# Performance work log

Measured on AMD Instinct MI355X. Metric: run time of the kernel, lower is better.

Reference implementation:

```python
import jax, jax.numpy as jnp
import numpy as np

B, K, N, M = 4, 512, 4096, 4
CHI2_95 = 7.815   # chi-square df=3, q=0.95
JITTER = 1e-6
ALPHA = 1.5       # sigma_cover_alpha
SIG_FLOOR = 1e-3
SIG_CEIL = 100.0
BETA = 0.85       # beta_parent_sigma
SHRINK = 1.0      # parent_sigma_shrink
KNN = 8           # fps_knn


def _sym(A):
    return 0.5 * (A + jnp.swapaxes(A, -1, -2))


def _chol3(S, eps=1e-6):
    # manual 3x3 Cholesky (vectorized, never fails), mirrors _safe_cholesky_3x3_manual
    s00, s11, s22 = S[..., 0, 0], S[..., 1, 1], S[..., 2, 2]
    s01, s02, s12 = S[..., 0, 1], S[..., 0, 2], S[..., 1, 2]
    l00 = jnp.sqrt(jnp.clip(s00, eps))
    l10 = s01 / jnp.clip(l00, eps)
    l20 = s02 / jnp.clip(l00, eps)
    l11 = jnp.sqrt(jnp.clip(s11 - l10 ** 2, eps))
    l21 = (s12 - l20 * l10) / jnp.clip(l11, eps)
    l22 = jnp.sqrt(jnp.clip(s22 - l20 ** 2 - l21 ** 2, eps))
    zz = jnp.zeros_like(l00)
    return jnp.stack([jnp.stack([l00, zz, zz], -1),
                      jnp.stack([l10, l11, zz], -1),
                      jnp.stack([l20, l21, l22], -1)], -2)


def _allocate_quota(pi, n_total, mask):
    # vectorized version of _allocate_quota: floor + largest-remainder
    valid = mask > 0.5
    pi = jnp.where(valid, pi, 0.0)
    pi = pi / jnp.clip(jnp.sum(pi, -1, keepdims=True), 1e-9)
    raw = pi * float(n_total)
    base = jnp.floor(raw)
    rem = (float(n_total) - jnp.sum(base, -1)).astype(jnp.int32)          # [B]
    frac = jnp.where(valid, raw - base, -1e9)
    order = jnp.argsort(-frac, axis=-1)
    rank = jnp.argsort(order, axis=-1)
    n_k = base.astype(jnp.int32) + (rank < rem[:, None]).astype(jnp.int32)
    return jnp.where(valid, n_k, 0)


def setup_inputs() -> dict:
    key = jax.random.key(0)
    k1, k2, k3, k4 = jax.random.split(key, 4)
    mu_p = jax.random.normal(k1, (B, K, 3), jnp.float32) * 5.0
    A = jax.random.normal(k2, (B, K, 3, 3), jnp.float32)
    Sig_p = 0.1 * jnp.einsum('bkij,bklj->bkil', A, A) + 0.5 * jnp.eye(3, dtype=jnp.float32)
    occ = jax.random.uniform(k3, (B, K), jnp.float32) + 0.1
    mask_parent = jnp.ones((B, K), jnp.float32)
    node_mask = jnp.ones((B, N), jnp.float32)
    z = jax.random.normal(k4, (B, N, M, 3), jnp.float32)
    return {"mu_p": mu_p, "Sig_p": Sig_p, "occ": occ,
            "mask_parent": mask_parent, "node_mask": node_mask, "z": z}


def reference(mu_p, Sig_p, occ, mask_parent, node_mask, z):
    b, k, _ = mu_p.shape
    n = node_mask.shape[1]
    m = z.shape[2]
    I3 = jnp.eye(3, dtype=mu_p.dtype)

    # --- quota allocation ---
    pi = occ * (mask_parent > 0.5).astype(occ.dtype)
    n_k = _allocate_quota(pi, n, mask_parent)                              # [B,K]

    # --- child -> parent assignment (packed layout, replaces Python loops) ---
    csum = jnp.cumsum(n_k, -1)                                             # [B,K]
    ar = jnp.arange(n)
    parent_idx = jax.vmap(lambda c: jnp.searchsorted(c, ar, side='right'))(csum)
    parent_idx = jnp.clip(parent_idx, 0, k - 1)                            # [B,N]

    # --- sample inside parent ellipsoid (rejection-lite) ---
    Sig_s = _sym(Sig_p * SHRINK) + JITTER * I3
    mu_c = jax.vmap(lambda a, i: a[i])(mu_p, parent_idx)                   # [B,N,3]
    Sig_c = jax.vmap(lambda a, i: a[i])(Sig_s, parent_idx)                 # [B,N,3,3]
    L = _chol3(Sig_c)                                                      # [B,N,3,3]
    cand = mu_c[:, :, None, :] + jnp.einsum('bnij,bnmj->bnmi', L, z)       # [B,N,M,3]
    # delta = cand - mu = L z, so maha2 = z^T z exactly (as in the torch code)
    maha2 = jnp.sum(z * z, -1)                                             # [B,N,M]
    inside = maha2 <= CHI2_95
    # keep first inside candidate; else smallest maha2
    score = jnp.where(inside, jnp.arange(m, dtype=maha2.dtype), 1e6 + maha2)
    pick = jnp.argmin(score, axis=-1)                                      # [B,N]
    mu0 = jnp.take_along_axis(cand, pick[..., None, None], axis=2)[:, :, 0, :]
    mu0 = mu0 * node_mask[..., None]                                       # [B,N,3]

    # --- spacing-based Sigma (kNN mean distance, isotropic) ---
    sq = jnp.sum(mu0 * mu0, -1)
    d2 = sq[:, :, None] + sq[:, None, :] - 2.0 * jnp.einsum('bnd,bmd->bnm', mu0, mu0)
    pair_ok = (node_mask[:, :, None] > 0.5) & (node_mask[:, None, :] > 0.5)
    eye = jnp.eye(n, dtype=bool)
    d2 = jnp.where(pair_ok & ~eye, d2, 1e9)
    neg_top, _ = jax.lax.top_k(-d2, KNN)                                   # [B,N,KNN]
    d_mean = jnp.mean(jnp.sqrt(jnp.clip(-neg_top, 0.0)), -1)               # [B,N]
    sigma = jnp.clip(ALPHA * d_mean, SIG_FLOOR, SIG_CEIL)
    Sig_spacing = (sigma ** 2)[..., None, None] * I3 + JITTER * I3         # [B,N,3,3]

    # --- parent/spacing Sigma blend ---
    Sig_pc = jax.vmap(lambda a, i: a[i])(_sym(Sig_p), parent_idx)
    Sig_pc = _sym(Sig_pc) + JITTER * I3
    Sig0 = BETA * Sig_pc + (1.0 - BETA) * Sig_spacing
    Sig0 = _sym(Sig0) + JITTER * I3
    Sig0 = Sig0 * node_mask[:, :, None, None]
    return mu0, Sig0, parent_idx
```

## Files before the change

### kernel.cpp

```cpp
#include <hip/hip_runtime.h>
#include <math.h>

#define B_ 4
#define K_ 512
#define N_ 4096
#define M_ 4

#define KTHREADS 512
#define SLOTS 8
#define SEGS 64
#define ROWS 16
#define CHUNK 1024
#define NCHUNK (N_ / CHUNK)
#define BIGF 3.0e38f

#define CSW(x,y) { float _lo = fminf(x,y); y = fmaxf(x,y); x = _lo; }

#define SORT8S(s0,s1,s2,s3,s4,s5,s6,s7) \
    CSW(s0,s1) CSW(s2,s3) CSW(s4,s5) CSW(s6,s7) \
    CSW(s0,s2) CSW(s1,s3) CSW(s4,s6) CSW(s5,s7) \
    CSW(s1,s2) CSW(s5,s6) \
    CSW(s0,s4) CSW(s1,s5) CSW(s2,s6) CSW(s3,s7) \
    CSW(s2,s4) CSW(s3,s5) \
    CSW(s1,s2) CSW(s3,s4) CSW(s5,s6)

#define BMERGE8S(K0,K1,K2,K3,K4,K5,K6,K7, S0,S1,S2,S3,S4,S5,S6,S7) \
    K0 = fminf(K0,S7); K1 = fminf(K1,S6); K2 = fminf(K2,S5); K3 = fminf(K3,S4); \
    K4 = fminf(K4,S3); K5 = fminf(K5,S2); K6 = fminf(K6,S1); K7 = fminf(K7,S0); \
    CSW(K0,K4) CSW(K1,K5) CSW(K2,K6) CSW(K3,K7) \
    CSW(K0,K2) CSW(K1,K3) CSW(K4,K6) CSW(K5,K7) \
    CSW(K0,K1) CSW(K2,K3) CSW(K4,K5) CSW(K6,K7)

#define WMERGE(K0,K1,K2,K3,K4,K5,K6,K7, off) { \
    float _b0 = __shfl_xor(K0, off, 64); float _b1 = __shfl_xor(K1, off, 64); \
    float _b2 = __shfl_xor(K2, off, 64); float _b3 = __shfl_xor(K3, off, 64); \
    float _b4 = __shfl_xor(K4, off, 64); float _b5 = __shfl_xor(K5, off, 64); \
    float _b6 = __shfl_xor(K6, off, 64); float _b7 = __shfl_xor(K7, off, 64); \
    BMERGE8S(K0,K1,K2,K3,K4,K5,K6,K7, _b0,_b1,_b2,_b3,_b4,_b5,_b6,_b7) }

__global__ __launch_bounds__(512) void fused_kernel(const float* __restrict__ mu_p,
                                                    const float* __restrict__ Sig_p,
                                                    const float* __restrict__ occ,
                                                    const float* __restrict__ mask_parent,
                                                    const float* __restrict__ node_mask,
                                                    const float* __restrict__ z,
                                                    float* __restrict__ out,
                                                    float4* __restrict__ mu4,
                                                    int useF4)
{
    __shared__ double sh_a[K_];
    __shared__ double sh_part[32];
    __shared__ alignas(16) double sh_frac[K_];
    __shared__ alignas(16) float  sh_ffr[K_];
    __shared__ float  csf[K_];
    __shared__ double Lsh[K_][6];
    __shared__ int    sh_wsum[8];
    __shared__ double s_S;
    __shared__ int    s_rem;

    int b  = blockIdx.x >> 3;
    int rb = blockIdx.x & 7;
    int k  = threadIdx.x;

    float mk = mask_parent[b * K_ + k];
    bool valid = mk > 0.5f;
    double pi = valid ? (double)occ[b * K_ + k] : 0.0;
    sh_a[k] = pi;
    __syncthreads();

    if (k < 32) {
        const double* a = sh_a + (k >> 3) * 128;
        int j = k & 7;
        double r = a[j];
        for (int i = 8; i < 128; i += 8) r += a[j + i];
        sh_part[k] = r;
    }
    __syncthreads();
    if (k == 0) {
        double pw[4];
        #pragma unroll
        for (int blk = 0; blk < 4; ++blk) {
            const double* p = sh_part + blk * 8;
            pw[blk] = ((p[0]+p[1])+(p[2]+p[3]))+((p[4]+p[5])+(p[6]+p[7]));
        }
        s_S = fmax((pw[0]+pw[1])+(pw[2]+pw[3]), 1e-9);
    }
    __syncthreads();

    double raw  = (pi / s_S) * 4096.0;
    double base = floor(raw);
    double frac = valid ? (raw - base) : -1e9;
    sh_frac[k] = frac;
    sh_ffr[k]  = (float)frac;
    __syncthreads();
    sh_a[k] = base;
    __syncthreads();
    if (k < 32) {
        const double* a = sh_a + (k >> 3) * 128;
        int j = k & 7;
        double r = a[j];
        for (int i = 8; i < 128; i += 8) r += a[j + i];
        sh_part[k] = r;
    }
    __syncthreads();
    if (k == 0) {
        double pw[4];
        #pragma unroll
        for (int blk = 0; blk < 4; ++blk) {
            const double* p = sh_part + blk * 8;
            pw[blk] = ((p[0]+p[1])+(p[2]+p[3]))+((p[4]+p[5])+(p[6]+p[7]));
        }
        s_rem = (int)(4096.0 - ((pw[0]+pw[1])+(pw[2]+pw[3])));
    }
    __syncthreads();

    int nkv = 0;
    if (valid) {
        float fl = (float)frac;
        int rank = 0, eq = 0;
        const float4* f4 = reinterpret_cast<const float4*>(sh_ffr);
        #pragma unroll 4
        for (int j4 = 0; j4 < K_ / 4; ++j4) {
            float4 q = f4[j4];
            rank += (q.x > fl) ? 1 : 0;  eq += (q.x == fl) ? 1 : 0;
            rank += (q.y > fl) ? 1 : 0;  eq += (q.y == fl) ? 1 : 0;
            rank += (q.z > fl) ? 1 : 0;  eq += (q.z == fl) ? 1 : 0;
            rank += (q.w > fl) ? 1 : 0;  eq += (q.w == fl) ? 1 : 0;
        }
        if (__builtin_expect(eq != 1, 0)) {
            double f = frac;
            rank = 0;
            for (int j = 0; j < K_; ++j) {
                double fj = sh_frac[j];
                rank += ((fj > f) || (fj == f && j < k)) ? 1 : 0;
            }
        }
        nkv = (int)base + (rank < s_rem ? 1 : 0);
    }

    {
        int lane = k & 63;
        int w    = k >> 6;
        int v = nkv;
        #pragma unroll
        for (int off = 1; off < 64; off <<= 1) {
            int t = __shfl_up(v, off, 64);
            v += (lane >= off) ? t : 0;
        }
        if (lane == 63) sh_wsum[w] = v;
        __syncthreads();
        int woff = 0;
        #pragma unroll
        for (int i = 0; i < 7; ++i) woff += (i < w) ? sh_wsum[i] : 0;
        csf[k] = (float)(v + woff);
    }

    {
        const float* S = Sig_p + (size_t)(b * K_ + k) * 9;
        double s00 = (double)S[0] + 1e-6;
        double s01 = 0.5 * ((double)S[1] + (double)S[3]);
        double s02 = 0.5 * ((double)S[2] + (double)S[6]);
        double s11 = (double)S[4] + 1e-6;
        double s12 = 0.5 * ((double)S[5] + (double)S[7]);
        double s22 = (double)S[8] + 1e-6;

        const double eps = 1e-6;
        double l00 = sqrt(fmax(s00, eps));
        double l10 = s01 / fmax(l00, eps);
        double l20 = s02 / fmax(l00, eps);
        double l11 = sqrt(fmax(s11 - l10 * l10, eps));
        double l21 = (s12 - l20 * l10) / fmax(l11, eps);
        double l22 = sqrt(fmax(s22 - l20 * l20 - l21 * l21, eps));

        Lsh[k][0] = l00; Lsh[k][1] = l10; Lsh[k][2] = l20;
        Lsh[k][3] = l11; Lsh[k][4] = l21; Lsh[k][5] = l22;
    }
    __syncthreads();

    int n = rb * 512 + k;
    float nf = (float)n;
    int lo = 0, hi = K_;
    while (lo < hi) {
        int mid = (lo + hi) >> 1;
        if (csf[mid] <= nf) lo = mid + 1; else hi = mid;
    }
    int p = lo < (K_ - 1) ? lo : (K_ - 1);

    double l00 = Lsh[p][0], l10 = Lsh[p][1], l20 = Lsh[p][2];
    double l11 = Lsh[p][3], l21 = Lsh[p][4], l22 = Lsh[p][5];

    const float* zp = z + (size_t)(b * N_ + n) * (M_ * 3);
    double bestScore = 1e30;
    int pick = 0;
    #pragma unroll
    for (int m = 0; m < M_; ++m) {
        double z0 = (double)zp[m*3+0], z1 = (double)zp[m*3+1], z2 = (double)zp[m*3+2];
        double maha2 = (z0 * z0 + z1 * z1) + z2 * z2;
        double score = (maha2 <= 7.815) ? (double)m : (1e6 + maha2);
        if (score < bestScore) { bestScore = score; pick = m; }
    }

    double z0 = (double)zp[pick*3+0], z1 = (double)zp[pick*3+1], z2 = (double)zp[pick*3+2];
    const float* mu = mu_p + (size_t)(b * K_ + p) * 3;
    double nm = (double)node_mask[b * N_ + n];
    double c0 = ((double)mu[0] + ((l00 * z0)))                       * nm;
    double c1 = ((double)mu[1] + ((l10 * z0 + l11 * z1)))            * nm;
    double c2 = ((double)mu[2] + ((l20 * z0 + l21 * z1) + l22 * z2)) * nm;

    size_t o = (size_t)(b * N_ + n) * 3;
    float f0 = (float)c0, f1 = (float)c1, f2 = (float)c2;
    out[o + 0] = f0;
    out[o + 1] = f1;
    out[o + 2] = f2;
    if (useF4) {
        float sq = (f0 * f0 + f1 * f1) + f2 * f2;
        mu4[b * N_ + n] = make_float4(f0, f1, f2, sq);
    }
    out[(size_t)B_ * N_ * 12 + (size_t)(b * N_ + n)] = (float)p;
}

#define LOADU_G(u, SQ) { \
    int col_ = colbase + u * SEGS + seg; \
    float4 q_ = cp[col_]; \
    s##u = fmaf(a00, q_.x, fmaf(a01, q_.y, fmaf(a02, q_.z, q_.w))); \
    r##u = fmaf(a10, q_.x, fmaf(a11, q_.y, fmaf(a12, q_.z, q_.w))); \
    if (SQ) { \
        s##u = (col_ == n0) ? BIGF : s##u; \
        r##u = (col_ == n1) ? BIGF : r##u; } }

#define LOADU_S(u, SQ) { \
    int col_ = colbase + u * SEGS + seg; \
    size_t o_ = (size_t)(bN + col_) * 3; \
    float qx_ = mu0[o_], qy_ = mu0[o_+1], qz_ = mu0[o_+2]; \
    float qw_ = (qx_*qx_ + qy_*qy_) + qz_*qz_; \
    s##u = fmaf(a00, qx_, fmaf(a01, qy_, fmaf(a02, qz_, qw_))); \
    r##u = fmaf(a10, qx_, fmaf(a11, qy_, fmaf(a12, qz_, qw_))); \
    if (SQ) { \
        s##u = (col_ == n0) ? BIGF : s##u; \
        r##u = (col_ == n1) ? BIGF : r##u; } }

#define GROUP8(LD, SQ) { \
    float s0,s1,s2,s3,s4,s5,s6,s7, r0,r1,r2,r3,r4,r5,r6,r7; \
    LD(0,SQ) LD(1,SQ) LD(2,SQ) LD(3,SQ) \
    LD(4,SQ) LD(5,SQ) LD(6,SQ) LD(7,SQ) \
    SORT8S(s0,s1,s2,s3,s4,s5,s6,s7) \
    BMERGE8S(ka0,ka1,ka2,ka3,ka4,ka5,ka6,ka7, s0,s1,s2,s3,s4,s5,s6,s7) \
    SORT8S(r0,r1,r2,r3,r4,r5,r6,r7) \
    BMERGE8S(kb0,kb1,kb2,kb3,kb4,kb5,kb6,kb7, r0,r1,r2,r3,r4,r5,r6,r7) }

__global__ __launch_bounds__(KTHREADS, 4) void knn_kernel(const float* __restrict__ Sig_p,
                                                          const float* __restrict__ node_mask,
                                                          const float4* __restrict__ mu4,
                                                          int useF4,
                                                          float* __restrict__ out)
{
    __shared__ float  shk[ROWS][8 * 8 + 1];

    int b   = blockIdx.x / (N_ / ROWS);
    int rb  = blockIdx.x % (N_ / ROWS);
    int tid = threadIdx.x;
    int slot = tid & (SLOTS - 1);
    int seg  = tid >> 3;

    const float* mu0 = out;
    const float4* cp = mu4 + (size_t)b * N_;
    int bN = b * N_;
    int n0 = rb * ROWS + slot;
    int n1 = n0 + SLOTS;

    float x0, y0, z0v, x1, y1, z1v;
    if (useF4) {
        float4 p0 = cp[n0]; x0 = p0.x; y0 = p0.y; z0v = p0.z;
        float4 p1 = cp[n1]; x1 = p1.x; y1 = p1.y; z1v = p1.z;
    } else {
        size_t so0 = (size_t)(bN + n0) * 3;
        size_t so1 = (size_t)(bN + n1) * 3;
        x0 = mu0[so0]; y0 = mu0[so0+1]; z0v = mu0[so0+2];
        x1 = mu0[so1]; y1 = mu0[so1+1]; z1v = mu0[so1+2];
    }
    float a00 = -2.0f*x0, a01 = -2.0f*y0, a02 = -2.0f*z0v;
    float a10 = -2.0f*x1, a11 = -2.0f*y1, a12 = -2.0f*z1v;

    float ka0=BIGF,ka1=BIGF,ka2=BIGF,ka3=BIGF,ka4=BIGF,ka5=BIGF,ka6=BIGF,ka7=BIGF;
    float kb0=BIGF,kb1=BIGF,kb2=BIGF,kb3=BIGF,kb4=BIGF,kb5=BIGF,kb6=BIGF,kb7=BIGF;

    int selfc = (rb * ROWS) >> 10;

    if (useF4) {
        #pragma unroll
        for (int c = 0; c < NCHUNK; ++c) {
            if (c == selfc) {
                { int colbase = c * CHUNK;       GROUP8(LOADU_G, 1) }
                { int colbase = c * CHUNK + 512; GROUP8(LOADU_G, 1) }
            } else {
                { int colbase = c * CHUNK;       GROUP8(LOADU_G, 0) }
                { int colbase = c * CHUNK + 512; GROUP8(LOADU_G, 0) }
            }
        }
    } else {
        #pragma unroll
        for (int c = 0; c < NCHUNK; ++c) {
            if (c == selfc) {
                { int colbase = c * CHUNK;       GROUP8(LOADU_S, 1) }
                { int colbase = c * CHUNK + 512; GROUP8(LOADU_S, 1) }
            } else {
                { int colbase = c * CHUNK;       GROUP8(LOADU_S, 0) }
                { int colbase = c * CHUNK + 512; GROUP8(LOADU_S, 0) }
            }
        }
    }

    WMERGE(ka0,ka1,ka2,ka3,ka4,ka5,ka6,ka7, 8)
    WMERGE(ka0,ka1,ka2,ka3,ka4,ka5,ka6,ka7, 16)
    WMERGE(ka0,ka1,ka2,ka3,ka4,ka5,ka6,ka7, 32)
    WMERGE(kb0,kb1,kb2,kb3,kb4,kb5,kb6,kb7, 8)
    WMERGE(kb0,kb1,kb2,kb3,kb4,kb5,kb6,kb7, 16)
    WMERGE(kb0,kb1,kb2,kb3,kb4,kb5,kb6,kb7, 32)

    int lane = tid & 63;
    int w    = tid >> 6;
    if (lane < SLOTS) {
        shk[lane][w*8+0] = ka0; shk[lane][w*8+1] = ka1;
        shk[lane][w*8+2] = ka2; shk[lane][w*8+3] = ka3;
        shk[lane][w*8+4] = ka4; shk[lane][w*8+5] = ka5;
        shk[lane][w*8+6] = ka6; shk[lane][w*8+7] = ka7;
        shk[lane+SLOTS][w*8+0] = kb0; shk[lane+SLOTS][w*8+1] = kb1;
        shk[lane+SLOTS][w*8+2] = kb2; shk[lane+SLOTS][w*8+3] = kb3;
        shk[lane+SLOTS][w*8+4] = kb4; shk[lane+SLOTS][w*8+5] = kb5;
        shk[lane+SLOTS][w*8+6] = kb6; shk[lane+SLOTS][w*8+7] = kb7;
    }
    __syncthreads();

    if (tid < ROWS) {
        int r = tid;
        int nn = rb * ROWS + r;
        float e0=BIGF,e1=BIGF,e2=BIGF,e3=BIGF,e4=BIGF,e5=BIGF,e6=BIGF,e7=BIGF;
        #pragma unroll
        for (int w2 = 0; w2 < 8; ++w2) {
            float b0 = shk[r][w2*8+0], b1 = shk[r][w2*8+1];
            float b2 = shk[r][w2*8+2], b3 = shk[r][w2*8+3];
            float b4 = shk[r][w2*8+4], b5 = shk[r][w2*8+5];
            float b6 = shk[r][w2*8+6], b7 = shk[r][w2*8+7];
            BMERGE8S(e0,e1,e2,e3,e4,e5,e6,e7, b0,b1,b2,b3,b4,b5,b6,b7)
        }

        float cn;
        if (useF4) {
            cn = cp[nn].w;
        } else {
            size_t so = (size_t)(bN + nn) * 3;
            float xx = mu0[so], yy = mu0[so+1], zz = mu0[so+2];
            cn = (xx*xx + yy*yy) + zz*zz;
        }

        double s0 = sqrt(fmax((double)(cn + e0), 0.0)), s1 = sqrt(fmax((double)(cn + e1), 0.0));
        double s2 = sqrt(fmax((double)(cn + e2), 0.0)), s3 = sqrt(fmax((double)(cn + e3), 0.0));
        double s4 = sqrt(fmax((double)(cn + e4), 0.0)), s5 = sqrt(fmax((double)(cn + e5), 0.0));
        double s6 = sqrt(fmax((double)(cn + e6), 0.0)), s7 = sqrt(fmax((double)(cn + e7), 0.0));
        double d_mean = (((s0 + s1) + (s2 + s3)) + ((s4 + s5) + (s6 + s7))) / 8.0;

        double sigma = fmin(fmax(1.5 * d_mean, 1e-3), 100.0);
        double spacing = sigma * sigma + 1e-6;

        int p = (int)out[(size_t)B_ * N_ * 12 + (size_t)(bN + nn)];
        const float* S = Sig_p + (size_t)(b * K_ + p) * 9;
        double s00 = (double)S[0];
        double s01 = 0.5 * ((double)S[1] + (double)S[3]);
        double s02 = 0.5 * ((double)S[2] + (double)S[6]);
        double s11 = (double)S[4];
        double s12 = 0.5 * ((double)S[5] + (double)S[7]);
        double s22 = (double)S[8];

        const double BETA = 0.85;
        const double OMB  = 1.0 - 0.85;
        double nm = (double)node_mask[bN + nn];

        double d00 = (BETA * (s00 + 1e-6) + OMB * spacing) + 1e-6;
        double d11 = (BETA * (s11 + 1e-6) + OMB * spacing) + 1e-6;
        double d22 = (BETA * (s22 + 1e-6) + OMB * spacing) + 1e-6;
        double o01 = BETA * s01;
        double o02 = BETA * s02;
        double o12 = BETA * s12;

        float* Sg = out + (size_t)B_ * N_ * 3 + (size_t)(bN + nn) * 9;
        Sg[0] = (float)(d00 * nm); Sg[1] = (float)(o01 * nm); Sg[2] = (float)(o02 * nm);
        Sg[3] = (float)(o01 * nm); Sg[4] = (float)(d11 * nm); Sg[5] = (float)(o12 * nm);
        Sg[6] = (float)(o02 * nm); Sg[7] = (float)(o12 * nm); Sg[8] = (float)(d22 * nm);
    }
}

extern "C" void kernel_launch(void* const* d_in, const int* in_sizes, int n_in,
                              void* d_out, int out_size, void* d_ws, size_t ws_size,
                              hipStream_t stream)
{
    const float* mu_p        = (const float*)d_in[0];
    const float* Sig_p       = (const float*)d_in[1];
    const float* occ         = (const float*)d_in[2];
    const float* mask_parent = (const float*)d_in[3];
    const float* node_mask   = (const float*)d_in[4];
    const float* z           = (const float*)d_in[5];
    float* out = (float*)d_out;

    int useF4 = (ws_size >= (size_t)B_ * N_ * sizeof(float4)) ? 1 : 0;
    float4* mu4 = (float4*)d_ws;

    fused_kernel<<<B_ * 8, 512, 0, stream>>>(mu_p, Sig_p, occ, mask_parent,
                                             node_mask, z, out, mu4, useF4);
    knn_kernel<<<B_ * (N_ / ROWS), KTHREADS, 0, stream>>>(Sig_p, node_mask,
                                                          mu4, useF4, out);
}
```

Before: 47.15 us.

## Process four query rows per thread in kNN kernel to reuse candidate loads

Each thread now keeps top-8 lists for four query points instead of two, so every float4 candidate load feeds four distance computations. This doubles rows per block and halves the block count. The chunk loop is no longer unrolled, probably to limit code size and register growth. The cost is higher register pressure from 32 running top-k registers plus temporaries, which may cut occupancy under launch_bounds(512,4) or cause spills, and fewer blocks reduce parallelism.

New measurement: 56.90 us. +20.7%, slower.

```diff
diff --git a/kernel.cpp b/kernel.cpp
--- a/kernel.cpp
+++ b/kernel.cpp
@@ -9,7 +9,7 @@
 #define KTHREADS 512
 #define SLOTS 8
 #define SEGS 64
-#define ROWS 16
+#define ROWSB 32
 #define CHUNK 1024
 #define NCHUNK (N_ / CHUNK)
 #define BIGF 3.0e38f
@@ -219,34 +219,49 @@
     out[(size_t)B_ * N_ * 12 + (size_t)(b * N_ + n)] = (float)p;
 }
 
-#define LOADU_G(u, SQ) { \
+#define LOADU4_G(u, SQ) { \
     int col_ = colbase + u * SEGS + seg; \
     float4 q_ = cp[col_]; \
-    s##u = fmaf(a00, q_.x, fmaf(a01, q_.y, fmaf(a02, q_.z, q_.w))); \
-    r##u = fmaf(a10, q_.x, fmaf(a11, q_.y, fmaf(a12, q_.z, q_.w))); \
+    qa##u = fmaf(a00, q_.x, fmaf(a01, q_.y, fmaf(a02, q_.z, q_.w))); \
+    qb##u = fmaf(a10, q_.x, fmaf(a11, q_.y, fmaf(a12, q_.z, q_.w))); \
+    qc##u = fmaf(a20, q_.x, fmaf(a21, q_.y, fmaf(a22, q_.z, q_.w))); \
+    qd##u = fmaf(a30, q_.x, fmaf(a31, q_.y, fmaf(a32, q_.z, q_.w))); \
     if (SQ) { \
-        s##u = (col_ == n0) ? BIGF : s##u; \
-        r##u = (col_ == n1) ? BIGF : r##u; } }
-
-#define LOADU_S(u, SQ) { \
+        qa##u = (col_ == n0) ? BIGF : qa##u; \
+        qb##u = (col_ == n1) ? BIGF : qb##u; \
+        qc##u = (col_ == n2) ? BIGF : qc##u; \
+        qd##u = (col_ == n3) ? BIGF : qd##u; } }
+
+#define LOADU4_S(u, SQ) { \
     int col_ = colbase + u * SEGS + seg; \
     size_t o_ = (size_t)(bN + col_) * 3; \
     float qx_ = mu0[o_], qy_ = mu0[o_+1], qz_ = mu0[o_+2]; \
     float qw_ = (qx_*qx_ + qy_*qy_) + qz_*qz_; \
-    s##u = fmaf(a00, qx_, fmaf(a01, qy_, fmaf(a02, qz_, qw_))); \
-    r##u = fmaf(a10, qx_, fmaf(a11, qy_, fmaf(a12, qz_, qw_))); \
+    qa##u = fmaf(a00, qx_, fmaf(a01, qy_, fmaf(a02, qz_, qw_))); \
+    qb##u = fmaf(a10, qx_, fmaf(a11, qy_, fmaf(a12, qz_, qw_))); \
+    qc##u = fmaf(a20, qx_, fmaf(a21, qy_, fmaf(a22, qz_, qw_))); \
+    qd##u = fmaf(a30, qx_, fmaf(a31, qy_, fmaf(a32, qz_, qw_))); \
     if (SQ) { \
-        s##u = (col_ == n0) ? BIGF : s##u; \
-        r##u = (col_ == n1) ? BIGF : r##u; } }
-
-#define GROUP8(LD, SQ) { \
-    float s0,s1,s2,s3,s4,s5,s6,s7, r0,r1,r2,r3,r4,r5,r6,r7; \
+        qa##u = (col_ == n0) ? BIGF : qa##u; \
+        qb##u = (col_ == n1) ? BIGF : qb##u; \
+        qc##u = (col_ == n2) ? BIGF : qc##u; \
+        qd##u = (col_ == n3) ? BIGF : qd##u; } }
+
+#define GROUP8R4(LD, SQ) { \
+    float qa0,qa1,qa2,qa3,qa4,qa5,qa6,qa7; \
+    float qb0,qb1,qb2,qb3,qb4,qb5,qb6,qb7; \
+    float qc0,qc1,qc2,qc3,qc4,qc5,qc6,qc7; \
+    float qd0,qd1,qd2,qd3,qd4,qd5,qd6,qd7; \
     LD(0,SQ) LD(1,SQ) LD(2,SQ) LD(3,SQ) \
     LD(4,SQ) LD(5,SQ) LD(6,SQ) LD(7,SQ) \
-    SORT8S(s0,s1,s2,s3,s4,s5,s6,s7) \
-    BMERGE8S(ka0,ka1,ka2,ka3,ka4,ka5,ka6,ka7, s0,s1,s2,s3,s4,s5,s6,s7) \
-    SORT8S(r0,r1,r2,r3,r4,r5,r6,r7) \
-    BMERGE8S(kb0,kb1,kb2,kb3,kb4,kb5,kb6,kb7, r0,r1,r2,r3,r4,r5,r6,r7) }
+    SORT8S(qa0,qa1,qa2,qa3,qa4,qa5,qa6,qa7) \
+    BMERGE8S(ka0,ka1,ka2,ka3,ka4,ka5,ka6,ka7, qa0,qa1,qa2,qa3,qa4,qa5,qa6,qa7) \
+    SORT8S(qb0,qb1,qb2,qb3,qb4,qb5,qb6,qb7) \
+    BMERGE8S(kb0,kb1,kb2,kb3,kb4,kb5,kb6,kb7, qb0,qb1,qb2,qb3,qb4,qb5,qb6,qb7) \
+    SORT8S(qc0,qc1,qc2,qc3,qc4,qc5,qc6,qc7) \
+    BMERGE8S(kc0,kc1,kc2,kc3,kc4,kc5,kc6,kc7, qc0,qc1,qc2,qc3,qc4,qc5,qc6,qc7) \
+    SORT8S(qd0,qd1,qd2,qd3,qd4,qd5,qd6,qd7) \
+    BMERGE8S(kd0,kd1,kd2,kd3,kd4,kd5,kd6,kd7, qd0,qd1,qd2,qd3,qd4,qd5,qd6,qd7) }
 
 __global__ __launch_bounds__(KTHREADS, 4) void knn_kernel(const float* __restrict__ Sig_p,
                                                           const float* __restrict__ node_mask,
@@ -254,10 +269,10 @@
                                                           int useF4,
                                                           float* __restrict__ out)
 {
-    __shared__ float  shk[ROWS][8 * 8 + 1];
-
-    int b   = blockIdx.x / (N_ / ROWS);
-    int rb  = blockIdx.x % (N_ / ROWS);
+    __shared__ float  shk[ROWSB][8 * 8 + 1];
+
+    int b   = blockIdx.x / (N_ / ROWSB);
+    int rb  = blockIdx.x % (N_ / ROWSB);
     int tid = threadIdx.x;
     int slot = tid & (SLOTS - 1);
     int seg  = tid >> 3;
@@ -265,47 +280,55 @@
     const float* mu0 = out;
     const float4* cp = mu4 + (size_t)b * N_;
     int bN = b * N_;
-    int n0 = rb * ROWS + slot;
+    int n0 = rb * ROWSB + slot;
     int n1 = n0 + SLOTS;
-
-    float x0, y0, z0v, x1, y1, z1v;
-    if (useF4) {
-        float4 p0 = cp[n0]; x0 = p0.x; y0 = p0.y; z0v = p0.z;
-        float4 p1 = cp[n1]; x1 = p1.x; y1 = p1.y; z1v = p1.z;
-    } else {
-        size_t so0 = (size_t)(bN + n0) * 3;
-        size_t so1 = (size_t)(bN + n1) * 3;
-        x0 = mu0[so0]; y0 = mu0[so0+1]; z0v = mu0[so0+2];
-        x1 = mu0[so1]; y1 = mu0[so1+1]; z1v = mu0[so1+2];
-    }
-    float a00 = -2.0f*x0, a01 = -2.0f*y0, a02 = -2.0f*z0v;
-    float a10 = -2.0f*x1, a11 = -2.0f*y1, a12 = -2.0f*z1v;
+    int n2 = n0 + 2 * SLOTS;
+    int n3 = n0 + 3 * SLOTS;
+
+    float a00,a01,a02, a10,a11,a12, a20,a21,a22, a30,a31,a32;
+    {
+        float x, y, zv;
+        if (useF4) { float4 p = cp[n0]; x = p.x; y = p.y; zv = p.z; }
+        else { size_t so = (size_t)(bN + n0) * 3; x = mu0[so]; y = mu0[so+1]; zv = mu0[so+2]; }
+        a00 = -2.0f*x; a01 = -2.0f*y; a02 = -2.0f*zv;
+        if (useF4) { float4 p = cp[n1]; x = p.x; y = p.y; zv = p.z; }
+        else { size_t so = (size_t)(bN + n1) * 3; x = mu0[so]; y = mu0[so+1]; zv = mu0[so+2]; }
+        a10 = -2.0f*x; a11 = -2.0f*y; a12 = -2.0f*zv;
+        if (useF4) { float4 p = cp[n2]; x = p.x; y = p.y; zv = p.z; }
+        else { size_t so = (size_t)(bN + n2) * 3; x = mu0[so]; y = mu0[so+1]; zv = mu0[so+2]; }
+        a20 = -2.0f*x; a21 = -2.0f*y; a22 = -2.0f*zv;
+        if (useF4) { float4 p = cp[n3]; x = p.x; y = p.y; zv = p.z; }
+        else { size_t so = (size_t)(bN + n3) * 3; x = mu0[so]; y = mu0[so+1]; zv = mu0[so+2]; }
+        a30 = -2.0f*x; a31 = -2.0f*y; a32 = -2.0f*zv;
+    }
 
     float ka0=BIGF,ka1=BIGF,ka2=BIGF,ka3=BIGF,ka4=BIGF,ka5=BIGF,ka6=BIGF,ka7=BIGF;
     float kb0=BIGF,kb1=BIGF,kb2=BIGF,kb3=BIGF,kb4=BIGF,kb5=BIGF,kb6=BIGF,kb7=BIGF;
-
-    int selfc = (rb * ROWS) >> 10;
+    float kc0=BIGF,kc1=BIGF,kc2=BIGF,kc3=BIGF,kc4=BIGF,kc5=BIGF,kc6=BIGF,kc7=BIGF;
+    float kd0=BIGF,kd1=BIGF,kd2=BIGF,kd3=BIGF,kd4=BIGF,kd5=BIGF,kd6=BIGF,kd7=BIGF;
+
+    int selfc = (rb * ROWSB) >> 10;
 
     if (useF4) {
-        #pragma unroll
+        #pragma unroll 1
         for (int c = 0; c < NCHUNK; ++c) {
             if (c == selfc) {
-                { int colbase = c * CHUNK;       GROUP8(LOADU_G, 1) }
-                { int colbase = c * CHUNK + 512; GROUP8(LOADU_G, 1) }
+                { int colbase = c * CHUNK;       GROUP8R4(LOADU4_G, 1) }
+                { int colbase = c * CHUNK + 512; GROUP8R4(LOADU4_G, 1) }
             } else {
-                { int colbase = c * CHUNK;       GROUP8(LOADU_G, 0) }
-                { int colbase = c * CHUNK + 512; GROUP8(LOADU_G, 0) }
+                { int colbase = c * CHUNK;       GROUP8R4(LOADU4_G, 0) }
+                { int colbase = c * CHUNK + 512; GROUP8R4(LOADU4_G, 0) }
             }
         }
     } else {
-        #pragma unroll
+        #pragma unroll 1
         for (int c = 0; c < NCHUNK; ++c) {
             if (c == selfc) {
-                { int colbase = c * CHUNK;       GROUP8(LOADU_S, 1) }
-                { int colbase = c * CHUNK + 512; GROUP8(LOADU_S, 1) }
+                { int colbase = c * CHUNK;       GROUP8R4(LOADU4_S, 1) }
+                { int colbase = c * CHUNK + 512; GROUP8R4(LOADU4_S, 1) }
             } else {
-                { int colbase = c * CHUNK;       GROUP8(LOADU_S, 0) }
-                { int colbase = c * CHUNK + 512; GROUP8(LOADU_S, 0) }
+                { int colbase = c * CHUNK;       GROUP8R4(LOADU4_S, 0) }
+                { int colbase = c * CHUNK + 512; GROUP8R4(LOADU4_S, 0) }
             }
         }
     }
@@ -316,24 +339,38 @@
     WMERGE(kb0,kb1,kb2,kb3,kb4,kb5,kb6,kb7, 8)
     WMERGE(kb0,kb1,kb2,kb3,kb4,kb5,kb6,kb7, 16)
     WMERGE(kb0,kb1,kb2,kb3,kb4,kb5,kb6,kb7, 32)
+    WMERGE(kc0,kc1,kc2,kc3,kc4,kc5,kc6,kc7, 8)
+    WMERGE(kc0,kc1,kc2,kc3,kc4,kc5,kc6,kc7, 16)
+    WMERGE(kc0,kc1,kc2,kc3,kc4,kc5,kc6,kc7, 32)
+    WMERGE(kd0,kd1,kd2,kd3,kd4,kd5,kd6,kd7, 8)
+    WMERGE(kd0,kd1,kd2,kd3,kd4,kd5,kd6,kd7, 16)
+    WMERGE(kd0,kd1,kd2,kd3,kd4,kd5,kd6,kd7, 32)
 
     int lane = tid & 63;
-    int w    = tid >> 6;
+    int wv   = tid >> 6;
     if (lane < SLOTS) {
-        shk[lane][w*8+0] = ka0; shk[lane][w*8+1] = ka1;
-        shk[lane][w*8+2] = ka2; shk[lane][w*8+3] = ka3;
-        shk[lane][w*8+4] = ka4; shk[lane][w*8+5] = ka5;
-        shk[lane][w*8+6] = ka6; shk[lane][w*8+7] = ka7;
-        shk[lane+SLOTS][w*8+0] = kb0; shk[lane+SLOTS][w*8+1] = kb1;
-        shk[lane+SLOTS][w*8+2] = kb2; shk[lane+SLOTS][w*8+3] = kb3;
-        shk[lane+SLOTS][w*8+4] = kb4; shk[lane+SLOTS][w*8+5] = kb5;
-        shk[lane+SLOTS][w*8+6] = kb6; shk[lane+SLOTS][w*8+7] = kb7;
-    }
-    __syncthreads();
-
-    if (tid < ROWS) {
+        shk[lane            ][wv*8+0] = ka0; shk[lane            ][wv*8+1] = ka1;
+        shk[lane            ][wv*8+2] = ka2; shk[lane            ][wv*8+3] = ka3;
+        shk[lane            ][wv*8+4] = ka4; shk[lane            ][wv*8+5] = ka5;
+        shk[lane            ][wv*8+6] = ka6; shk[lane            ][wv*8+7] = ka7;
+        shk[lane +     SLOTS][wv*8+0] = kb0; shk[lane +     SLOTS][wv*8+1] = kb1;
+        shk[lane +     SLOTS][wv*8+2] = kb2; shk[lane +     SLOTS][wv*8+3] = kb3;
+        shk[lane +     SLOTS][wv*8+4] = kb4; shk[lane +     SLOTS][wv*8+5] = kb5;
+        shk[lane +     SLOTS][wv*8+6] = kb6; shk[lane +     SLOTS][wv*8+7] = kb7;
+        shk[lane + 2 * SLOTS][wv*8+0] = kc0; shk[lane + 2 * SLOTS][wv*8+1] = kc1;
+        shk[lane + 2 * SLOTS][wv*8+2] = kc2; shk[lane + 2 * SLOTS][wv*8+3] = kc3;
+        shk[lane + 2 * SLOTS][wv*8+4] = kc4; shk[lane + 2 * SLOTS][wv*8+5] = kc5;
+        shk[lane + 2 * SLOTS][wv*8+6] = kc6; shk[lane + 2 * SLOTS][wv*8+7] = kc7;
+        shk[lane + 3 * SLOTS][wv*8+0] = kd0; shk[lane + 3 * SLOTS][wv*8+1] = kd1;
+        shk[lane + 3 * SLOTS][wv*8+2] = kd2; shk[lane + 3 * SLOTS][wv*8+3] = kd3;
+        shk[lane + 3 * SLOTS][wv*8+4] = kd4; shk[lane + 3 * SLOTS][wv*8+5] = kd5;
+        shk[lane + 3 * SLOTS][wv*8+6] = kd6; shk[lane + 3 * SLOTS][wv*8+7] = kd7;
+    }
+    __syncthreads();
+
+    if (tid < ROWSB) {
         int r = tid;
-        int nn = rb * ROWS + r;
+        int nn = rb * ROWSB + r;
         float e0=BIGF,e1=BIGF,e2=BIGF,e3=BIGF,e4=BIGF,e5=BIGF,e6=BIGF,e7=BIGF;
         #pragma unroll
         for (int w2 = 0; w2 < 8; ++w2) {
@@ -406,6 +443,6 @@
 
     fused_kernel<<<B_ * 8, 512, 0, stream>>>(mu_p, Sig_p, occ, mask_parent,
                                              node_mask, z, out, mu4, useF4);
-    knn_kernel<<<B_ * (N_ / ROWS), KTHREADS, 0, stream>>>(Sig_p, node_mask,
-                                                          mu4, useF4, out);
+    knn_kernel<<<B_ * (N_ / ROWSB), KTHREADS, 0, stream>>>(Sig_p, node_mask,
+                                                           mu4, useF4, out);
 }
```
